# Kernel optimization log

Measured on AMD Instinct MI355X. Metric: run time of the kernel, lower is better.

The kernel has to match this reference:

```python
import jax, jax.numpy as jnp
import numpy as np

B, F, C = 64, 256, 100000
T = 1.0           # temperature t
P_MARGIN = 0.2    # positive margin
N_MARGIN = 0.3    # negative margin


def setup_inputs() -> dict:
    key = jax.random.key(0)
    k1, k2, k3, k4, k5 = jax.random.split(key, 5)
    inputs = jax.random.normal(k1, (B, F), jnp.float32)
    targets = jax.random.randint(k2, (B,), 0, C)
    pos_mask = jax.random.bernoulli(k3, 0.1, (B, B))
    neg_mask = jax.random.bernoulli(k4, 0.3, (B, B))
    V = jax.random.normal(k5, (C, F), jnp.float32)
    V = V / jnp.linalg.norm(V, axis=1, keepdims=True)  # bank rows are L2-normalized
    return {"inputs": inputs, "targets": targets, "pos_mask": pos_mask,
            "neg_mask": neg_mask, "V": V}


def _masked_bce_ones(vals, mask):
    # F.binary_cross_entropy_with_logits(vals[mask], ones) == mean softplus(-vals[mask]);
    # returns 0 when no entry is selected (matches the hpsims.shape[0]==0 branch).
    cnt = mask.sum()
    s = jnp.sum(jnp.where(mask, jax.nn.softplus(-vals), 0.0))
    return jnp.where(cnt > 0, s / jnp.maximum(cnt, 1).astype(vals.dtype), 0.0)


def reference(inputs, targets, pos_mask, neg_mask, V):
    # Exclusive.forward: memory-bank lookup GEMM, scaled by t
    logits = (inputs @ V.T) * T                       # [B, C]
    bu_loss = -jnp.take_along_axis(jax.nn.log_softmax(logits, axis=1),
                                   targets[:, None], axis=1).mean()

    # masked pairwise similarity hard-mining loss
    x = inputs / jnp.linalg.norm(inputs, axis=1, keepdims=True)
    sims = jnp.clip(x @ x.T, -1.0, 1.0)               # [B, B]
    offdiag = ~jnp.eye(B, dtype=bool)                 # original drops the diagonal

    psims = jnp.where(pos_mask, sims, 2.0)            # 2.0 = sentinel for non-pairs
    nsims = jnp.where(neg_mask, sims, 2.0)

    # n_thrds: per-row min of psims (off-diag) minus n_margin
    n_thrds = jnp.where(offdiag, psims, jnp.inf).min(axis=1, keepdims=True) - N_MARGIN
    # p_thrds: sentinels flipped to -2, then per-row max minus p_margin
    thd = jnp.where(psims == 2.0, -2.0, psims)
    p_thrds = jnp.where(offdiag, thd, -jnp.inf).max(axis=1, keepdims=True) - P_MARGIN

    hp_loss = _masked_bce_ones(psims, offdiag & (psims < p_thrds))
    hn_loss = _masked_bce_ones(nsims, offdiag & (nsims < n_thrds))

    loss = bu_loss + hp_loss + hn_loss
    return (loss, logits)
```

## Files before the change

### kernel.cpp

```cpp
#include <hip/hip_runtime.h>
#include <math.h>

#define FF 256
#define CC 100000
#define PMARG 0.2f
#define NMARG 0.3f
#define NB2 3125
#define W_A 0
#define W_GRAM 8192
#define W_SE 12288
#define W_PART 12352

typedef __attribute__((ext_vector_type(8))) short short8;
typedef __attribute__((ext_vector_type(4))) float f32x4;

__device__ __forceinline__ float wredf(float v) {
#pragma unroll
    for (int s = 1; s < 64; s <<= 1) v += __shfl_xor(v, s, 64);
    return v;
}
__device__ __forceinline__ short f2bf(float f) {
    unsigned u = __float_as_uint(f);
    unsigned r = (u + 0x7fffu + ((u >> 16) & 1u)) >> 16;
    return (short)r;
}
__device__ __forceinline__ short8 pack8(float4 a, float4 b) {
    short8 o;
    o[0] = f2bf(a.x); o[1] = f2bf(a.y); o[2] = f2bf(a.z); o[3] = f2bf(a.w);
    o[4] = f2bf(b.x); o[5] = f2bf(b.y); o[6] = f2bf(b.z); o[7] = f2bf(b.w);
    return o;
}
__device__ __forceinline__ float dot4(float4 a, float4 b) {
    return a.x * b.x + a.y * b.y + a.z * b.z + a.w * b.w;
}

__global__ __launch_bounds__(256) void k_prep(const float* __restrict__ in,
                                              float* __restrict__ ws) {
    int tid = threadIdx.x;
    int b = blockIdx.x;
    const float4* __restrict__ in4 = (const float4*)in;
    if (b == 4) {
        short8* __restrict__ wsa = (short8*)(ws + W_A);
#pragma unroll
        for (int i = 0; i < 8; ++i) {
            int idx = i * 256 + tid;
            int lane = idx & 63;
            int ks = (idx >> 6) & 7;
            int mt = idx >> 9;
            int row = mt * 16 + (lane & 15);
            int kq = ks * 8 + (lane >> 4) * 2;
            wsa[idx] = pack8(in4[row * 64 + kq], in4[row * 64 + kq + 1]);
        }
        return;
    }
    __shared__ float4 sIn[64 * 64];
#pragma unroll
    for (int i = 0; i < 16; ++i) sIn[i * 256 + tid] = in4[i * 256 + tid];
    __syncthreads();
    int qr = b >> 1, qc = b & 1;
    int r0 = qr * 32 + (tid >> 4) * 2;
    int c0 = qc * 32 + (tid & 15) * 2;
    float g00 = 0.f, g01 = 0.f, g10 = 0.f, g11 = 0.f;
    for (int kq = 0; kq < 64; ++kq) {
        float4 a0 = sIn[(r0 + 0) * 64 + kq];
        float4 a1 = sIn[(r0 + 1) * 64 + kq];
        float4 b0 = sIn[(c0 + 0) * 64 + kq];
        float4 b1 = sIn[(c0 + 1) * 64 + kq];
        g00 += dot4(a0, b0); g01 += dot4(a0, b1);
        g10 += dot4(a1, b0); g11 += dot4(a1, b1);
    }
    float* G = ws + W_GRAM;
    G[(r0 + 0) * 64 + c0 + 0] = g00;
    G[(r0 + 0) * 64 + c0 + 1] = g01;
    G[(r0 + 1) * 64 + c0 + 0] = g10;
    G[(r0 + 1) * 64 + c0 + 1] = g11;
}

__global__ __launch_bounds__(256, 2) void k_gemm2f(const float* __restrict__ V,
                                                   const float* __restrict__ ws_in,
                                                   float* __restrict__ logits,
                                                   float* __restrict__ ws) {
    __shared__ float sW[64][2];
    int tid = threadIdx.x;
    int lane = tid & 63, w = tid >> 6;
    int ctl = w & 1, rh = w >> 1;
    int ct = blockIdx.x * 2 + ctl;
    int g = lane >> 4, c4 = lane & 15;
    int col = ct * 16 + c4;

    const float4* __restrict__ vp =
        (const float4*)V + (size_t)(ct * 16 + c4) * 64 + g * 2;
    float4 b0a = vp[0],  b0b = vp[1];
    float4 b1a = vp[8],  b1b = vp[9];
    float4 b2a = vp[16], b2b = vp[17];
    float4 b3a = vp[24], b3b = vp[25];
    float4 b4a = vp[32], b4b = vp[33];
    float4 b5a = vp[40], b5b = vp[41];
    float4 b6a = vp[48], b6b = vp[49];
    float4 b7a = vp[56], b7b = vp[57];
    __builtin_amdgcn_sched_barrier(0);

    const short8* __restrict__ ap =
        (const short8*)(ws_in + W_A) + (size_t)rh * 16 * 64 + lane;

    f32x4 acc0 = {0.f, 0.f, 0.f, 0.f};
    f32x4 acc1 = {0.f, 0.f, 0.f, 0.f};
#define GSTEP(K, BA, BB)                                                     \
    {                                                                        \
        short8 bf = pack8(BA, BB);                                           \
        short8 a0 = ap[K * 64];                                              \
        short8 a1 = ap[(8 + K) * 64];                                        \
        acc0 = __builtin_amdgcn_mfma_f32_16x16x32_bf16(a0, bf, acc0, 0, 0, 0);\
        acc1 = __builtin_amdgcn_mfma_f32_16x16x32_bf16(a1, bf, acc1, 0, 0, 0);\
    }
    GSTEP(0, b0a, b0b)
    GSTEP(1, b1a, b1b)
    GSTEP(2, b2a, b2b)
    GSTEP(3, b3a, b3b)
    GSTEP(4, b4a, b4b)
    GSTEP(5, b5a, b5b)
    GSTEP(6, b6a, b6b)
    GSTEP(7, b7a, b7b)
#undef GSTEP

#pragma unroll
    for (int q = 0; q < 2; ++q) {
        f32x4 a = q ? acc1 : acc0;
#pragma unroll
        for (int r = 0; r < 4; ++r) {
            int row = rh * 32 + q * 16 + g * 4 + r;
            float lg = a[r];
            logits[(size_t)row * CC + col] = lg;
            float e = expf(lg);
            e += __shfl_xor(e, 1, 64); e += __shfl_xor(e, 2, 64);
            e += __shfl_xor(e, 4, 64); e += __shfl_xor(e, 8, 64);
            if (c4 == 0) sW[row][ctl] = e;
        }
    }
    __syncthreads();
    if (tid < 64)
        ws[W_PART + (size_t)blockIdx.x * 64 + tid] = sW[tid][0] + sW[tid][1];
}

__global__ __launch_bounds__(256) void k_comb(const float* __restrict__ ws_in,
                                              float* __restrict__ ws) {
    __shared__ float sS[256];
    int row = blockIdx.x;
    int tid = threadIdx.x;
    const float* __restrict__ P = ws_in + W_PART;
    float s = 0.f;
    for (int b = tid; b < NB2; b += 256) s += P[(size_t)b * 64 + row];
    sS[tid] = s;
    __syncthreads();
    if (tid < 128) sS[tid] += sS[tid + 128];
    __syncthreads();
    if (tid < 64) {
        float v = sS[tid] + sS[tid + 64];
        v = wredf(v);
        if (tid == 0) ws[W_SE + row] = v;
    }
}

__device__ __forceinline__ bool mask_at(const void* p, int idx, int mode) {
    if (mode == 0) return ((const int*)p)[idx] != 0;
    if (mode == 1) return ((const float*)p)[idx] != 0.f;
    return ((const unsigned char*)p)[idx] != 0;
}

__global__ __launch_bounds__(256) void k_final(const int* __restrict__ targets,
                                               const void* __restrict__ pmask,
                                               const void* __restrict__ nmask,
                                               const float* __restrict__ logits,
                                               const float* __restrict__ ws,
                                               float* __restrict__ out) {
    __shared__ float sG[4096];
    __shared__ char sPM[16384];
    __shared__ char sNM[16384];
    __shared__ int sMode;
    int tid = threadIdx.x;

    float myLogit = 0.f, mySe = 0.f;
    if (tid < 64) {
        int tgt = targets[tid];
        myLogit = logits[(size_t)tid * CC + tgt];
        mySe = ws[W_SE + tid];
    }
    {
        const float4* __restrict__ G4 = (const float4*)(ws + W_GRAM);
        float4* sG4 = (float4*)sG;
#pragma unroll
        for (int i = 0; i < 4; ++i) sG4[tid + i * 256] = G4[tid + i * 256];
    }
    if (tid < 64) {
        const unsigned int* pw = (const unsigned int*)pmask;
        int okInt = 1, okFlt = 1;
#pragma unroll
        for (int i = 0; i < 16; ++i) {
            unsigned int wv = pw[tid * 16 + i];
            okInt = okInt && (wv <= 1u);
            okFlt = okFlt && (wv == 0u || wv == 0x3f800000u);
        }
        int mode = __all(okInt) ? 0 : (__all(okFlt) ? 1 : 2);
        if (tid == 0) sMode = mode;
    }
    __syncthreads();
    int mode = sMode;
    int mq = (mode == 2) ? 256 : 1024;
    for (int i = tid; i < mq; i += 256) {
        ((float4*)sPM)[i] = ((const float4*)pmask)[i];
        ((float4*)sNM)[i] = ((const float4*)nmask)[i];
    }
    __syncthreads();
    if (tid >= 64) return;

    int lane = tid;
    float lse = logf(mySe);
    float nll = lse - myLogit;

    float rinv = rsqrtf(sG[lane * 64 + lane]);

    float minp = INFINITY, maxthd = -INFINITY;
    for (int j = 0; j < 64; ++j) {
        float rj = __shfl(rinv, j, 64);
        float sim = sG[lane * 64 + j] * rinv * rj;
        sim = fminf(1.f, fmaxf(-1.f, sim));
        if (j != lane) {
            bool pm = mask_at(sPM, lane * 64 + j, mode);
            float ps = pm ? sim : 2.0f;
            minp = fminf(minp, ps);
            maxthd = fmaxf(maxthd, pm ? sim : -2.0f);
        }
    }
    float n_thrd = minp - NMARG;
    float p_thrd = maxthd - PMARG;

    float hps = 0.f, hns = 0.f, hpc = 0.f, hnc = 0.f;
    for (int j = 0; j < 64; ++j) {
        float rj = __shfl(rinv, j, 64);
        float sim = sG[lane * 64 + j] * rinv * rj;
        sim = fminf(1.f, fmaxf(-1.f, sim));
        if (j != lane) {
            bool pm = mask_at(sPM, lane * 64 + j, mode);
            bool nm = mask_at(sNM, lane * 64 + j, mode);
            float ps = pm ? sim : 2.0f;
            float ns = nm ? sim : 2.0f;
            if (ps < p_thrd) { hps += log1pf(expf(-ps)); hpc += 1.f; }
            if (ns < n_thrd) { hns += log1pf(expf(-ns)); hnc += 1.f; }
        }
    }

    float snll = wredf(nll);
    float shps = wredf(hps);
    float shns = wredf(hns);
    float shpc = wredf(hpc);
    float shnc = wredf(hnc);
    if (lane == 0) {
        float bu = snll * (1.f / 64.f);
        float hp = shpc > 0.f ? shps / shpc : 0.f;
        float hn = shnc > 0.f ? shns / shnc : 0.f;
        out[0] = bu + hp + hn;
    }
}

extern "C" void kernel_launch(void* const* d_in, const int* in_sizes, int n_in,
                              void* d_out, int out_size, void* d_ws, size_t ws_size,
                              hipStream_t stream) {
    const float* inputs = (const float*)d_in[0];
    const int* targets  = (const int*)d_in[1];
    const void* pmask   = d_in[2];
    const void* nmask   = d_in[3];
    const float* V      = (const float*)d_in[4];
    float* out = (float*)d_out;
    float* logits = out + 1;
    float* ws = (float*)d_ws;

    hipLaunchKernelGGL(k_prep, dim3(5), dim3(256), 0, stream, inputs, ws);
    hipLaunchKernelGGL(k_gemm2f, dim3(NB2), dim3(256), 0, stream,
                       V, ws, logits, ws);
    hipLaunchKernelGGL(k_comb, dim3(64), dim3(256), 0, stream, ws, ws);
    hipLaunchKernelGGL(k_final, dim3(1), dim3(256), 0, stream,
                       targets, pmask, nmask, logits, ws, out);
}
```

Baseline: 102.0 us.

## Give each wave all 64 rows of a 16-column tile, load V nontemporally

Before, the GEMM kernel split each 16-column tile of V across two waves, each handling 32 rows, so every V row was loaded and converted to bf16 twice. Now each wave covers all 64 batch rows with four MFMA accumulators, so each V element is read and packed once. The grid shrinks to 1563 blocks with a bounds guard for the leftover tile. The per-block shared-memory reduction and __syncthreads are dropped: each wave writes its own partial exp-sums, and the combine kernel reads twice as many partials. V loads become nontemporal to avoid polluting the cache. This trades more accumulator registers and more partial-sum traffic for halving the V reads and conversions.

```diff
diff --git a/kernel.cpp b/kernel.cpp
--- a/kernel.cpp
+++ b/kernel.cpp
@@ -5,7 +5,9 @@
 #define CC 100000
 #define PMARG 0.2f
 #define NMARG 0.3f
-#define NB2 3125
+#define NB3 1563
+#define NCT 6250
+#define NPART (NB3 * 4)
 #define W_A 0
 #define W_GRAM 8192
 #define W_SE 12288
@@ -28,6 +30,12 @@
     short8 o;
     o[0] = f2bf(a.x); o[1] = f2bf(a.y); o[2] = f2bf(a.z); o[3] = f2bf(a.w);
     o[4] = f2bf(b.x); o[5] = f2bf(b.y); o[6] = f2bf(b.z); o[7] = f2bf(b.w);
+    return o;
+}
+__device__ __forceinline__ short8 pack8v(f32x4 a, f32x4 b) {
+    short8 o;
+    o[0] = f2bf(a[0]); o[1] = f2bf(a[1]); o[2] = f2bf(a[2]); o[3] = f2bf(a[3]);
+    o[4] = f2bf(b[0]); o[5] = f2bf(b[1]); o[6] = f2bf(b[2]); o[7] = f2bf(b[3]);
     return o;
 }
 __device__ __forceinline__ float dot4(float4 a, float4 b) {
@@ -76,42 +84,51 @@
     G[(r0 + 1) * 64 + c0 + 1] = g11;
 }
 
-__global__ __launch_bounds__(256, 2) void k_gemm2f(const float* __restrict__ V,
-                                                   const float* __restrict__ ws_in,
-                                                   float* __restrict__ logits,
-                                                   float* __restrict__ ws) {
-    __shared__ float sW[64][2];
+__global__ __launch_bounds__(256, 2) void k_gemm3(const float* __restrict__ V,
+                                                  const float* __restrict__ ws_in,
+                                                  float* __restrict__ logits,
+                                                  float* __restrict__ ws) {
     int tid = threadIdx.x;
     int lane = tid & 63, w = tid >> 6;
-    int ctl = w & 1, rh = w >> 1;
-    int ct = blockIdx.x * 2 + ctl;
+    int ct = blockIdx.x * 4 + w;
     int g = lane >> 4, c4 = lane & 15;
-    int col = ct * 16 + c4;
-
-    const float4* __restrict__ vp =
-        (const float4*)V + (size_t)(ct * 16 + c4) * 64 + g * 2;
-    float4 b0a = vp[0],  b0b = vp[1];
-    float4 b1a = vp[8],  b1b = vp[9];
-    float4 b2a = vp[16], b2b = vp[17];
-    float4 b3a = vp[24], b3b = vp[25];
-    float4 b4a = vp[32], b4b = vp[33];
-    float4 b5a = vp[40], b5b = vp[41];
-    float4 b6a = vp[48], b6b = vp[49];
-    float4 b7a = vp[56], b7b = vp[57];
+    bool ctv = ct < NCT;
+    int vr = ctv ? (ct * 16 + c4) : (CC - 1);
+
+    const f32x4* __restrict__ vp = (const f32x4*)V + (size_t)vr * 64 + g * 2;
+    f32x4 b0a = __builtin_nontemporal_load(vp + 0);
+    f32x4 b0b = __builtin_nontemporal_load(vp + 1);
+    f32x4 b1a = __builtin_nontemporal_load(vp + 8);
+    f32x4 b1b = __builtin_nontemporal_load(vp + 9);
+    f32x4 b2a = __builtin_nontemporal_load(vp + 16);
+    f32x4 b2b = __builtin_nontemporal_load(vp + 17);
+    f32x4 b3a = __builtin_nontemporal_load(vp + 24);
+    f32x4 b3b = __builtin_nontemporal_load(vp + 25);
+    f32x4 b4a = __builtin_nontemporal_load(vp + 32);
+    f32x4 b4b = __builtin_nontemporal_load(vp + 33);
+    f32x4 b5a = __builtin_nontemporal_load(vp + 40);
+    f32x4 b5b = __builtin_nontemporal_load(vp + 41);
+    f32x4 b6a = __builtin_nontemporal_load(vp + 48);
+    f32x4 b6b = __builtin_nontemporal_load(vp + 49);
+    f32x4 b7a = __builtin_nontemporal_load(vp + 56);
+    f32x4 b7b = __builtin_nontemporal_load(vp + 57);
     __builtin_amdgcn_sched_barrier(0);
 
-    const short8* __restrict__ ap =
-        (const short8*)(ws_in + W_A) + (size_t)rh * 16 * 64 + lane;
-
-    f32x4 acc0 = {0.f, 0.f, 0.f, 0.f};
-    f32x4 acc1 = {0.f, 0.f, 0.f, 0.f};
-#define GSTEP(K, BA, BB)                                                     \
-    {                                                                        \
-        short8 bf = pack8(BA, BB);                                           \
-        short8 a0 = ap[K * 64];                                              \
-        short8 a1 = ap[(8 + K) * 64];                                        \
-        acc0 = __builtin_amdgcn_mfma_f32_16x16x32_bf16(a0, bf, acc0, 0, 0, 0);\
-        acc1 = __builtin_amdgcn_mfma_f32_16x16x32_bf16(a1, bf, acc1, 0, 0, 0);\
+    const short8* __restrict__ ap = (const short8*)(ws_in + W_A) + lane;
+
+    f32x4 acc[4];
+#pragma unroll
+    for (int mt = 0; mt < 4; ++mt) acc[mt] = (f32x4){0.f, 0.f, 0.f, 0.f};
+
+#define GSTEP(K, BA, BB)                                                      \
+    {                                                                         \
+        short8 bf = pack8v(BA, BB);                                           \
+        _Pragma("unroll")                                                     \
+        for (int mt = 0; mt < 4; ++mt) {                                      \
+            short8 a = ap[(mt * 8 + K) * 64];          \
+            acc[mt] = __builtin_amdgcn_mfma_f32_16x16x32_bf16(a, bf, acc[mt], \
+                                                              0, 0, 0);       \
+        }                                                                     \
     }
     GSTEP(0, b0a, b0b)
     GSTEP(1, b1a, b1b)
@@ -123,23 +140,20 @@
     GSTEP(7, b7a, b7b)
 #undef GSTEP
 
-#pragma unroll
-    for (int q = 0; q < 2; ++q) {
-        f32x4 a = q ? acc1 : acc0;
+    int col = ct * 16 + c4;
+    float* __restrict__ P = ws + W_PART + (size_t)(blockIdx.x * 4 + w) * 64;
+#pragma unroll
+    for (int mt = 0; mt < 4; ++mt)
 #pragma unroll
         for (int r = 0; r < 4; ++r) {
-            int row = rh * 32 + q * 16 + g * 4 + r;
-            float lg = a[r];
-            logits[(size_t)row * CC + col] = lg;
-            float e = expf(lg);
+            int row = mt * 16 + g * 4 + r;
+            float lg = acc[mt][r];
+            if (ctv) logits[(size_t)row * CC + col] = lg;
+            float e = ctv ? expf(lg) : 0.f;
             e += __shfl_xor(e, 1, 64); e += __shfl_xor(e, 2, 64);
             e += __shfl_xor(e, 4, 64); e += __shfl_xor(e, 8, 64);
-            if (c4 == 0) sW[row][ctl] = e;
-        }
-    }
-    __syncthreads();
-    if (tid < 64)
-        ws[W_PART + (size_t)blockIdx.x * 64 + tid] = sW[tid][0] + sW[tid][1];
+            if (c4 == 0) P[row] = e;
+        }
 }
 
 __global__ __launch_bounds__(256) void k_comb(const float* __restrict__ ws_in,
@@ -149,7 +163,7 @@
     int tid = threadIdx.x;
     const float* __restrict__ P = ws_in + W_PART;
     float s = 0.f;
-    for (int b = tid; b < NB2; b += 256) s += P[(size_t)b * 64 + row];
+    for (int b = tid; b < NPART; b += 256) s += P[(size_t)b * 64 + row];
     sS[tid] = s;
     __syncthreads();
     if (tid < 128) sS[tid] += sS[tid + 128];
@@ -275,7 +289,7 @@
     float* ws = (float*)d_ws;
 
     hipLaunchKernelGGL(k_prep, dim3(5), dim3(256), 0, stream, inputs, ws);
-    hipLaunchKernelGGL(k_gemm2f, dim3(NB2), dim3(256), 0, stream,
+    hipLaunchKernelGGL(k_gemm3, dim3(NB3), dim3(256), 0, stream,
                        V, ws, logits, ws);
     hipLaunchKernelGGL(k_comb, dim3(64), dim3(256), 0, stream, ws, ws);
     hipLaunchKernelGGL(k_final, dim3(1), dim3(256), 0, stream,
```

Result: slower. 107.3 us (+5.2%).
